# Optimization experiments

Hardware: AMD Instinct MI355X
Metric: run time of the kernel (lower is better)

Reference implementation:

```python
import jax, jax.numpy as jnp
import numpy as np

N_HEADS = 8
THETA = 10000.0
T2 = 8  # hard-coded local window sizes from the source
F2 = 8


def _rope(x, theta=THETA):
    # x: (b, h, n, d). lucidrains RotaryEmbedding convention: interleaved pairs,
    # freqs repeated '(f 2)', rotate_half on adjacent pairs.
    n, d = x.shape[-2], x.shape[-1]
    inv_freq = 1.0 / (theta ** (jnp.arange(0, d, 2, dtype=jnp.float32) / d))  # (d/2,)
    ang = jnp.arange(n, dtype=jnp.float32)[:, None] * inv_freq               # (n, d/2)
    ang = jnp.repeat(ang, 2, axis=-1)                                        # (n, d)
    cos, sin = jnp.cos(ang).astype(x.dtype), jnp.sin(ang).astype(x.dtype)
    xp = x.reshape(*x.shape[:-1], d // 2, 2)
    xr = jnp.stack([-xp[..., 1], xp[..., 0]], axis=-1).reshape(x.shape)
    return x * cos + xr * sin


def _sdpa(q, k, v):
    # non-causal scaled dot-product attention, scale = 1/sqrt(head_dim)
    d = q.shape[-1]
    s = jnp.einsum('bhqd,bhkd->bhqk', q, k) / jnp.sqrt(jnp.asarray(d, q.dtype))
    return jnp.einsum('bhqk,bhkd->bhqd', jax.nn.softmax(s, axis=-1), v)


def _attend(x, W, h):
    # x: (b, n, D); W: (D, 3D) pre-transposed Linear weight. RoPE on q and k.
    b, n, D = x.shape
    qkv = (x @ W).reshape(b, n, 3, h, D // h).transpose(2, 0, 3, 1, 4)  # (3,b,h,n,hd)
    q, k, v = _rope(qkv[0]), _rope(qkv[1]), qkv[2]
    o = _sdpa(q, k, v)  # (b, h, n, hd)
    return o.transpose(0, 2, 1, 3).reshape(b, n, D)


def reference(x, W1, W2, W3, Wp):
    B, D, T, F = x.shape
    h = N_HEADS
    # stage 1: attention along time axis, independent per (batch, freq)
    xt = x.transpose(0, 3, 2, 1).reshape(B * F, T, D)   # 'b d t f -> (b f) t d'
    xt = _attend(xt, W1, h)
    # stage 2: attention along freq axis, independent per (batch, time)
    xf = xt.reshape(B, F, T, D).transpose(0, 2, 1, 3).reshape(B * T, F, D)
    xf = _attend(xf, W2, h)
    t1, f1 = T // T2, F // F2
    xw = xf.reshape(B, t1, T2, f1, F2, D).transpose(0, 1, 3, 2, 4, 5)
    xw = xw.reshape(B * t1 * f1, T2 * F2, D)
    xw = _attend(xw, W3, h)
    y = xw.reshape(B, t1, f1, T2, F2, D).transpose(0, 1, 3, 2, 4, 5).reshape(B, T, F, D)
    y = y @ Wp                                          # c_proj, no bias
    return y.transpose(0, 3, 1, 2)                      # 'b t f d -> b d t f'


def setup_inputs() -> dict:
    key = jax.random.key(0)
    B, D, T, F = 4, 256, 256, 64
    ks = jax.random.split(key, 5)
    s = 1.0 / np.sqrt(D)
    return {
        'x': jax.random.normal(ks[0], (B, D, T, F), dtype=jnp.float32),
        'W1': jax.random.normal(ks[1], (D, 3 * D), dtype=jnp.float32) * s,
        'W2': jax.random.normal(ks[2], (D, 3 * D), dtype=jnp.float32) * s,
        'W3': jax.random.normal(ks[3], (D, 3 * D), dtype=jnp.float32) * s,
        'Wp': jax.random.normal(ks[4], (D, D), dtype=jnp.float32) * s,
    }
```

## Files before the change

### kernel.cpp

```cpp
#include <hip/hip_runtime.h>
#include <math.h>

#define B_  4
#define D_  256
#define T_  256
#define F_  64
#define H_  8

#define LN10000 9.210340371976184f
#define SM_SCALE 0.17677669529663687f
#define LOG2E    1.4426950408889634f

typedef float f32x4  __attribute__((ext_vector_type(4)));
typedef float f32x16 __attribute__((ext_vector_type(16)));
typedef short s16x8  __attribute__((ext_vector_type(8)));

__device__ __forceinline__ unsigned short f2bf(float x) {
    unsigned u = __float_as_uint(x);
    return (unsigned short)((u + 0x7fffu + ((u >> 16) & 1u)) >> 16);
}
__device__ __forceinline__ float bf2f(unsigned short h) {
    return __uint_as_float(((unsigned)h) << 16);
}
__device__ __forceinline__ int cvt_pk_bf16(float a, float b) {
    int r;
    asm("v_cvt_pk_bf16_f32 %0, %1, %2" : "=v"(r) : "v"(a), "v"(b));
    return r;
}
__device__ __forceinline__ float exp2fast(float x) {
    float r;
    asm("v_exp_f32 %0, %1" : "=v"(r) : "v"(x));
    return r;
}

__device__ __forceinline__ int xcd_swz(int lin, int nwg) {
    return (lin & 7) * (nwg >> 3) + (lin >> 3);
}

#define GLOAD_LDS(g, l)                                                         \
    __builtin_amdgcn_global_load_lds(                                           \
        (const __attribute__((address_space(1))) void*)(g),                     \
        (__attribute__((address_space(3))) void*)(l), 16, 0, 0)

__global__ __launch_bounds__(256) void rope_table(float2* __restrict__ tab) {
    const int idx = blockIdx.x * 256 + threadIdx.x;
    const int pos = idx >> 4, pr = idx & 15;
    const float freq = __expf(-(float)(2 * pr) * (LN10000 / 32.0f));
    float s, c;
    __sincosf((float)pos * freq, &s, &c);
    tab[idx] = make_float2(c, s);
}

__global__ __launch_bounds__(256) void split_w(const float* __restrict__ W,
                                               char* __restrict__ img, int N) {
    __shared__ float Wt[64][132];
    const int nb = blockIdx.x, ks = blockIdx.y;
    const int tid = threadIdx.x;
#pragma unroll
    for (int j = 0; j < 8; ++j) {
        int idx = j * 1024 + tid * 4;
        int r = idx >> 7, cidx = idx & 127;
        const float4 v = *reinterpret_cast<const float4*>(
            &W[(size_t)(ks * 64 + r) * N + nb * 128 + cidx]);
        Wt[r][cidx] = v.x; Wt[r][cidx + 1] = v.y;
        Wt[r][cidx + 2] = v.z; Wt[r][cidx + 3] = v.w;
    }
    __syncthreads();
    char* base = img + ((size_t)(nb * 4 + ks)) * 32768;
#pragma unroll
    for (int i = 0; i < 4; ++i) {
        int p = i * 256 + tid;
        int n = p >> 3, seg = p & 7;
        s16x8 hi, lo;
#pragma unroll
        for (int e = 0; e < 8; ++e) {
            float v = Wt[seg * 8 + e][n];
            unsigned short hb = f2bf(v);
            hi[e] = (short)hb;
            lo[e] = (short)f2bf(v - bf2f(hb));
        }
        int off = n * 128 + ((seg * 16) ^ ((n & 7) << 4));
        *(s16x8*)(base + off) = hi;
        *(s16x8*)(base + 16384 + off) = lo;
    }
}

__global__ __launch_bounds__(256) void transpose_in(const float* __restrict__ x,
                                                    char* __restrict__ Ximg) {
    __shared__ float tile[32][33];
    const int bt = blockIdx.z, b = bt >> 8, t = bt & 255;
    const int d0 = blockIdx.x * 32, f0 = blockIdx.y * 32;
    const int tx = threadIdx.x, ty = threadIdx.y;
    const size_t xbase = (size_t)b * D_ * T_ * F_ + (size_t)t * F_;
#pragma unroll
    for (int j = 0; j < 4; ++j) {
        int d = d0 + ty + j * 8;
        tile[ty + j * 8][tx] = x[xbase + (size_t)d * T_ * F_ + f0 + tx];
    }
    __syncthreads();
    const int tok = (b * 64 + f0 + tx) * 256 + t;
    const int rloc = tok & 127;
    const int hl = ty >> 2, seg = ty & 3;
    if (hl) return;
    char* base = Ximg + ((size_t)((tok >> 7) * 4 + (d0 >> 6))) * 32768;
    const int off = rloc * 128 + ((((d0 & 32) << 1) + seg * 16) ^ ((rloc & 7) << 4));
    s16x8 v;
#pragma unroll
    for (int e = 0; e < 8; ++e) v[e] = (short)f2bf(tile[seg * 8 + e][tx]);
    *(s16x8*)(base + off) = v;
}

__global__ __launch_bounds__(256) void gemm_x2(const char* __restrict__ Aimg,
                                               const char* __restrict__ Bimg,
                                               unsigned short* __restrict__ C, int N) {
    __shared__ alignas(16) char lds[49152];
    const int tid = threadIdx.x, lane = tid & 63, wave = tid >> 6;
    const int wm = wave >> 1, wn = wave & 1;
    const int rlo = lane & 15, rg = lane >> 4;
    const int wg = xcd_swz(blockIdx.x, gridDim.x);
    const int ncol = N >> 7;
    const int brow = wg / ncol, bcol = wg % ncol;
    f32x4 acc[4][4] = {};
    for (int ks = 0; ks < 4; ++ks) {
        const char* ga = Aimg + ((size_t)(brow * 4 + ks)) * 32768 + wave * 4096 + lane * 16;
        const char* gb = Bimg + ((size_t)(bcol * 4 + ks)) * 32768 + wave * 8192 + lane * 16;
#pragma unroll
        for (int i = 0; i < 4; ++i)
            GLOAD_LDS(ga + i * 1024, lds + wave * 4096 + lane * 16 + i * 1024);
#pragma unroll
        for (int i = 0; i < 8; ++i)
            GLOAD_LDS(gb + i * 1024, lds + 16384 + wave * 8192 + lane * 16 + i * 1024);
        __syncthreads();
#pragma unroll
        for (int kk = 0; kk < 2; ++kk) {
            s16x8 ah[4], bh[4], bl[4];
#pragma unroll
            for (int i = 0; i < 4; ++i) {
                const int ra = wm * 64 + i * 16 + rlo;
                const int ka = (kk * 64 + rg * 16) ^ ((ra & 7) << 4);
                ah[i] = *(const s16x8*)(lds + ra * 128 + ka);
                const int rb = wn * 64 + i * 16 + rlo;
                const int kb = (kk * 64 + rg * 16) ^ ((rb & 7) << 4);
                bh[i] = *(const s16x8*)(lds + 16384 + rb * 128 + kb);
                bl[i] = *(const s16x8*)(lds + 32768 + rb * 128 + kb);
            }
#pragma unroll
            for (int mt = 0; mt < 4; ++mt)
#pragma unroll
                for (int nt = 0; nt < 4; ++nt) {
                    acc[mt][nt] = __builtin_amdgcn_mfma_f32_16x16x32_bf16(ah[mt], bh[nt], acc[mt][nt], 0, 0, 0);
                    acc[mt][nt] = __builtin_amdgcn_mfma_f32_16x16x32_bf16(ah[mt], bl[nt], acc[mt][nt], 0, 0, 0);
                }
        }
        __syncthreads();
    }
    const int row0 = brow * 128 + wm * 64, col0 = bcol * 128 + wn * 64;
#pragma unroll
    for (int mt = 0; mt < 4; ++mt)
#pragma unroll
        for (int nt = 0; nt < 4; ++nt)
#pragma unroll
            for (int r = 0; r < 4; ++r)
                C[(size_t)(row0 + mt * 16 + rg * 4 + r) * N + col0 + nt * 16 + rlo] =
                    f2bf(acc[mt][nt][r]);
}

__global__ __launch_bounds__(256) void gemm_cproj(const char* __restrict__ Aimg,
                                                  const char* __restrict__ Bimg,
                                                  float* __restrict__ out, int tok0) {
    __shared__ alignas(16) char lds[65536];
    const int tid = threadIdx.x, lane = tid & 63, wave = tid >> 6;
    const int wm = wave >> 1, wn = wave & 1;
    const int rlo = lane & 15, rg = lane >> 4;
    const int wg = xcd_swz(blockIdx.x, gridDim.x);
    const int brow = wg >> 1, bcol = wg & 1;
    f32x4 acc[4][4] = {};
    for (int ks = 0; ks < 4; ++ks) {
        const char* ga = Aimg + ((size_t)(brow * 4 + ks)) * 32768 + wave * 8192 + lane * 16;
        const char* gb = Bimg + ((size_t)(bcol * 4 + ks)) * 32768 + wave * 8192 + lane * 16;
        char* la = lds + wave * 8192;
        char* lb = lds + 32768 + wave * 8192;
#pragma unroll
        for (int i = 0; i < 8; ++i) {
            GLOAD_LDS(ga + i * 1024, la + lane * 16 + i * 1024);
            GLOAD_LDS(gb + i * 1024, lb + lane * 16 + i * 1024);
        }
        __syncthreads();
#pragma unroll
        for (int kk = 0; kk < 2; ++kk) {
            s16x8 ah[4], al[4], bh[4], bl[4];
#pragma unroll
            for (int i = 0; i < 4; ++i) {
                const int ra = wm * 64 + i * 16 + rlo;
                const int ka = (kk * 64 + rg * 16) ^ ((ra & 7) << 4);
                ah[i] = *(const s16x8*)(lds + ra * 128 + ka);
                al[i] = *(const s16x8*)(lds + 16384 + ra * 128 + ka);
                const int rb = wn * 64 + i * 16 + rlo;
                const int kb = (kk * 64 + rg * 16) ^ ((rb & 7) << 4);
                bh[i] = *(const s16x8*)(lds + 32768 + rb * 128 + kb);
                bl[i] = *(const s16x8*)(lds + 49152 + rb * 128 + kb);
            }
#pragma unroll
            for (int mt = 0; mt < 4; ++mt)
#pragma unroll
                for (int nt = 0; nt < 4; ++nt) {
                    acc[mt][nt] = __builtin_amdgcn_mfma_f32_16x16x32_bf16(ah[mt], bh[nt], acc[mt][nt], 0, 0, 0);
                    acc[mt][nt] = __builtin_amdgcn_mfma_f32_16x16x32_bf16(ah[mt], bl[nt], acc[mt][nt], 0, 0, 0);
                    acc[mt][nt] = __builtin_amdgcn_mfma_f32_16x16x32_bf16(al[mt], bh[nt], acc[mt][nt], 0, 0, 0);
                }
        }
        __syncthreads();
    }
    float* ct = (float*)lds;
#pragma unroll
    for (int mt = 0; mt < 4; ++mt)
#pragma unroll
        for (int nt = 0; nt < 4; ++nt)
#pragma unroll
            for (int r = 0; r < 4; ++r) {
                const int tok = wm * 64 + mt * 16 + rg * 4 + r;
                const int d   = wn * 64 + nt * 16 + rlo;
                ct[d * 128 + (tok ^ ((d & 7) << 2))] = acc[mt][nt][r];
            }
    __syncthreads();
    const int tokb = tok0 + brow * 128;
    const int bidx = tokb >> 14;
    const int t0 = (tokb >> 6) & 255;
    const int dcol0 = bcol * 128;
#pragma unroll
    for (int it = 0; it < 16; ++it) {
        const int seg = it * 16 + (tid >> 4);
        const int dd = seg >> 1, tt = seg & 1;
        const int f0 = (tid & 15) * 4;
        const float4 v = *(const float4*)&ct[dd * 128 + ((tt * 64 + f0) ^ ((dd & 7) << 2))];
        *(float4*)&out[((size_t)((bidx * 256 + dcol0 + dd) * 256 + t0 + tt)) * 64 + f0] = v;
    }
}

template <int STAGE, bool WLO>
__global__ __launch_bounds__(256) void attn_mfma(const unsigned short* __restrict__ qkv,
                                                 char* __restrict__ Ximg,
                                                 const float2* __restrict__ ropeT, int s0) {
    constexpr int L   = (STAGE == 1) ? 256 : 64;
    constexpr int HPB = (STAGE == 1) ? 1 : 2;
    constexpr int GX  = (STAGE == 1) ? 8 : 4;
    constexpr int NCH = L / 32;
    constexpr int KVB = L * 64;
    __shared__ alignas(16) char kvLds[HPB * 2 * KVB];
    __shared__ alignas(16) float Osc[4][32][36];
    const int tid = threadIdx.x, lane = tid & 63, wave = tid >> 6;
    const int hiSel = lane >> 5;
    const int qloc = lane & 31;
    const int wg = xcd_swz(blockIdx.x, gridDim.x);
    const int hx = wg & (GX - 1);
    const int sl = wg / GX;
    float* PL = &Osc[wave][0][0];

    {
        const int nIter = (STAGE == 1) ? 2 : 1;
#pragma unroll
        for (int it = 0; it < nIter; ++it) {
            int idx, headl;
            if (STAGE == 1) { idx = it * 256 + tid; headl = 0; }
            else            { idx = tid & 127;      headl = tid >> 7; }
            const int k = idx >> 1, dh = idx & 1;
            const int h = hx * HPB + headl;
            const size_t grow = ((size_t)(sl * L + k)) * 768 + h * 32 + dh * 16;
            const s16x8 kr0 = *(const s16x8*)&qkv[grow + 256];
            const s16x8 kr1 = *(const s16x8*)&qkv[grow + 264];
            const s16x8 vr0 = *(const s16x8*)&qkv[grow + 512];
            const s16x8 vr1 = *(const s16x8*)&qkv[grow + 520];
            float kvv[16];
#pragma unroll
            for (int e = 0; e < 8; ++e) {
                kvv[e]     = bf2f((unsigned short)kr0[e]);
                kvv[8 + e] = bf2f((unsigned short)kr1[e]);
            }
#pragma unroll
            for (int j = 0; j < 8; ++j) {
                const float2 cs = ropeT[k * 16 + dh * 8 + j];
                const float x0 = kvv[2 * j], x1 = kvv[2 * j + 1];
                kvv[2 * j]     = x0 * cs.x - x1 * cs.y;
                kvv[2 * j + 1] = x1 * cs.x + x0 * cs.y;
            }
            char* kf = kvLds + headl * 2 * KVB;
            s16x8 wlo, whi;
#pragma unroll
            for (int e = 0; e < 8; ++e) {
                wlo[e] = (short)f2bf(kvv[e]);
                whi[e] = (short)f2bf(kvv[8 + e]);
            }
            *(s16x8*)(kf + (((k >> 5) * 2 + dh) * 64 + (k & 31)) * 16) = wlo;
            *(s16x8*)(kf + (((k >> 5) * 2 + dh) * 64 + 32 + (k & 31)) * 16) = whi;
            char* vf = kf + KVB;
            const int kb = k >> 4, hi8 = (k >> 3) & 1, eo = (k & 7) * 2;
#pragma unroll
            for (int dp = 0; dp < 16; ++dp) {
                const unsigned short vv = (unsigned short)((dp < 8) ? vr0[dp] : vr1[dp - 8]);
                *(unsigned short*)(vf + (kb * 64 + dh * 16 + dp + 32 * hi8) * 16 + eo) = vv;
            }
        }
    }
    __syncthreads();

    const int headl = (STAGE == 1) ? 0 : (wave >> 1);
    const int h = hx * HPB + headl;
    const char* Kf = kvLds + headl * 2 * KVB;
    const char* Vf = Kf + KVB;
    const int nPass = (STAGE == 1) ? 2 : 1;
    const float QS = SM_SCALE * LOG2E;
    const float THR = 8.0f * LOG2E;

    for (int pass = 0; pass < nPass; ++pass) {
        const int qt = (STAGE == 1) ? (wave + pass * 4) : (wave & 1);
        const int q = qt * 32 + qloc;
        s16x8 qf0, qf1;
        {
            const size_t qrow = ((size_t)(sl * L + q)) * 768 + h * 32;
            const s16x8 qr0 = *(const s16x8*)&qkv[qrow + hiSel * 8];
            const s16x8 qr1 = *(const s16x8*)&qkv[qrow + 16 + hiSel * 8];
#pragma unroll
            for (int j = 0; j < 4; ++j) {
                const float2 c0 = ropeT[q * 16 + hiSel * 4 + j];
                const float a0 = bf2f((unsigned short)qr0[2 * j]);
                const float a1 = bf2f((unsigned short)qr0[2 * j + 1]);
                qf0[2 * j]     = (short)f2bf((a0 * c0.x - a1 * c0.y) * QS);
                qf0[2 * j + 1] = (short)f2bf((a1 * c0.x + a0 * c0.y) * QS);
                const float2 c1 = ropeT[q * 16 + 8 + hiSel * 4 + j];
                const float b0 = bf2f((unsigned short)qr1[2 * j]);
                const float b1 = bf2f((unsigned short)qr1[2 * j + 1]);
                qf1[2 * j]     = (short)f2bf((b0 * c1.x - b1 * c1.y) * QS);
                qf1[2 * j + 1] = (short)f2bf((b1 * c1.x + b0 * c1.y) * QS);
            }
        }
        f32x16 o = (f32x16)0.0f;
        float m = -INFINITY, lsum = 0.f;
#pragma unroll
        for (int c = 0; c < NCH; ++c) {
            const s16x8 ka = *(const s16x8*)(Kf + (c * 2 + 0) * 1024 + lane * 16);
            const s16x8 kb = *(const s16x8*)(Kf + (c * 2 + 1) * 1024 + lane * 16);
            f32x16 S = (f32x16)0.0f;
            S = __builtin_amdgcn_mfma_f32_32x32x16_bf16(ka, qf0, S, 0, 0, 0);
            S = __builtin_amdgcn_mfma_f32_32x32x16_bf16(kb, qf1, S, 0, 0, 0);
            float cmax = S[0];
#pragma unroll
            for (int r = 1; r < 16; ++r) cmax = fmaxf(cmax, S[r]);
            cmax = fmaxf(cmax, __shfl_xor(cmax, 32, 64));
            if (__any(cmax > m + THR)) {
                const float mnew = fmaxf(m, cmax);
                const float corr = exp2fast(m - mnew);
                m = mnew;
                lsum *= corr;
#pragma unroll
                for (int r = 0; r < 16; ++r) o[r] *= corr;
            }
            float p[16], ssum = 0.f;
#pragma unroll
            for (int r = 0; r < 16; ++r) { p[r] = exp2fast(S[r] - m); ssum += p[r]; }
            lsum += ssum;
#pragma unroll
            for (int j = 0; j < 8; ++j)
                PL[((j & 1) + 4 * (j >> 1) + 2 * hiSel) * 32 + qloc] =
                    __int_as_float(cvt_pk_bf16(p[2 * j], p[2 * j + 1]));
            union { int u[4]; s16x8 v; } P0, P1;
#pragma unroll
            for (int i = 0; i < 4; ++i) {
                P0.u[i] = __float_as_int(PL[(hiSel * 4 + i) * 32 + qloc]);
                P1.u[i] = __float_as_int(PL[(8 + hiSel * 4 + i) * 32 + qloc]);
            }
            const s16x8 va = *(const s16x8*)(Vf + (c * 2 + 0) * 1024 + lane * 16);
            const s16x8 vb = *(const s16x8*)(Vf + (c * 2 + 1) * 1024 + lane * 16);
            o = __builtin_amdgcn_mfma_f32_32x32x16_bf16(va, P0.v, o, 0, 0, 0);
            o = __builtin_amdgcn_mfma_f32_32x32x16_bf16(vb, P1.v, o, 0, 0, 0);
        }
        lsum += __shfl_xor(lsum, 32, 64);
        const float inv = 1.0f / lsum;
#pragma unroll
        for (int r = 0; r < 16; ++r)
            Osc[wave][qloc][(r & 3) + 8 * (r >> 2) + 4 * hiSel] = o[r] * inv;
        int tok;
        if constexpr (STAGE == 1) {
            const int s = s0 + sl, b = s >> 6, f = s & 63;
            tok = (b * 256 + q) * 64 + f;
        } else if constexpr (STAGE == 2) {
            const int s2 = s0 + sl, b = s2 >> 8, t = s2 & 255;
            tok = ((b * 32 + (t >> 3)) * 8 + (q >> 3)) * 64 + (t & 7) * 8 + (q & 7);
        } else {
            const int w = s0 + sl, b = w >> 8, tb = (w >> 3) & 31, fb = w & 7;
            tok = (b * 256 + tb * 8 + (q >> 3)) * 64 + fb * 8 + (q & 7);
        }
        const int rloc = tok & 127;
        char* base = Ximg + ((size_t)((tok >> 7) * 4 + (h >> 1))) * 32768;
        const int sw = (rloc & 7) << 4;
        const int hb64 = (h & 1) * 64;
#pragma unroll
        for (int gg = 0; gg < 2; ++gg) {
            const int g = hiSel * 2 + gg;
            float v8[8];
            *(float4*)&v8[0] = *(const float4*)&Osc[wave][qloc][g * 8];
            *(float4*)&v8[4] = *(const float4*)&Osc[wave][qloc][g * 8 + 4];
            const int off = rloc * 128 + ((hb64 + g * 16) ^ sw);
            s16x8 hi;
#pragma unroll
            for (int e = 0; e < 8; ++e) hi[e] = (short)f2bf(v8[e]);
            *(s16x8*)(base + off) = hi;
            if constexpr (WLO) {
                s16x8 lo;
#pragma unroll
                for (int e = 0; e < 8; ++e)
                    lo[e] = (short)f2bf(v8[e] - bf2f((unsigned short)hi[e]));
                *(s16x8*)(base + 16384 + off) = lo;
            }
        }
    }
}

extern "C" void kernel_launch(void* const* d_in, const int* in_sizes, int n_in,
                              void* d_out, int out_size, void* d_ws, size_t ws_size,
                              hipStream_t stream) {
    const float* x  = (const float*)d_in[0];
    const float* W1 = (const float*)d_in[1];
    const float* W2 = (const float*)d_in[2];
    const float* W3 = (const float*)d_in[3];
    const float* Wp = (const float*)d_in[4];
    float* out = (float*)d_out;

    const size_t M = (size_t)B_ * T_ * F_;
    char* Xa = (char*)d_out;
    char* Xb = (char*)d_ws;
    char* W1i = (char*)d_ws + M * 1024;
    char* W2i = W1i + 786432;
    char* W3i = W2i + 786432;
    char* Wpi = W3i + 786432;
    float2* ropeT = (float2*)(Wpi + 262144);
    unsigned short* qkvB = (unsigned short*)((char*)ropeT + 32768);

    const size_t fixedBytes = M * 1024 + 3 * 786432 + 262144 + 32768;
    int CH = 2048;
    const int cands[5] = {65536, 32768, 16384, 8192, 4096};
    for (int i = 0; i < 5; ++i) {
        if (fixedBytes + (size_t)cands[i] * 1536 <= ws_size) { CH = cands[i]; break; }
    }
    const int NC = (int)(M / CH);

    rope_table<<<16, 256, 0, stream>>>(ropeT);
    split_w<<<dim3(6, 4), 256, 0, stream>>>(W1, W1i, 768);
    split_w<<<dim3(6, 4), 256, 0, stream>>>(W2, W2i, 768);
    split_w<<<dim3(6, 4), 256, 0, stream>>>(W3, W3i, 768);
    split_w<<<dim3(2, 4), 256, 0, stream>>>(Wp, Wpi, 256);

    transpose_in<<<dim3(8, 2, 1024), dim3(32, 8), 0, stream>>>(x, Xa);

    for (int c = 0; c < NC; ++c) {
        gemm_x2<<<(CH / 128) * 6, 256, 0, stream>>>(
            Xa + (size_t)c * CH * 1024, W1i, qkvB, 768);
        attn_mfma<1, false><<<8 * (CH / 256), 256, 0, stream>>>(
            qkvB, Xb, ropeT, c * (CH / 256));
    }
    for (int c = 0; c < NC; ++c) {
        gemm_x2<<<(CH / 128) * 6, 256, 0, stream>>>(
            Xb + (size_t)c * CH * 1024, W2i, qkvB, 768);
        attn_mfma<2, false><<<4 * (CH / 64), 256, 0, stream>>>(
            qkvB, Xa, ropeT, c * (CH / 64));
    }
    for (int c = 0; c < NC; ++c) {
        gemm_x2<<<(CH / 128) * 6, 256, 0, stream>>>(
            Xa + (size_t)c * CH * 1024, W3i, qkvB, 768);
        attn_mfma<3, true><<<4 * (CH / 64), 256, 0, stream>>>(
            qkvB, Xb, ropeT, c * (CH / 64));
    }
    for (int c = 0; c < NC; ++c) {
        gemm_cproj<<<(CH / 128) * 2, 256, 0, stream>>>(
            Xb + (size_t)c * CH * 1024, Wpi, out, c * CH);
    }
}
```

Measured before the change: 359.5 us.

## Store QKV in per-sequence head-section layout and tree-reduce softmax max/sum

The QKV GEMM epilogue now writes its output in a [seq][head][q/k/v][token][32] layout instead of row-major 768-wide rows, and the attention kernels read Q, K and V from those contiguous per-head sections. This aims to make attention loads contiguous per head and sequence, improving cache-line use. The GEMM stores become scattered 2-byte writes with more index arithmetic. Separately, the row max and row sum over 16 score values become balanced trees to shorten the dependency chain.

```diff
diff --git a/kernel.cpp b/kernel.cpp
--- a/kernel.cpp
+++ b/kernel.cpp
@@ -31,6 +31,23 @@
     float r;
     asm("v_exp_f32 %0, %1" : "=v"(r) : "v"(x));
     return r;
+}
+__device__ __forceinline__ float max16(const f32x16& S) {
+    float a0 = fmaxf(S[0], S[1]),  a1 = fmaxf(S[2], S[3]);
+    float a2 = fmaxf(S[4], S[5]),  a3 = fmaxf(S[6], S[7]);
+    float a4 = fmaxf(S[8], S[9]),  a5 = fmaxf(S[10], S[11]);
+    float a6 = fmaxf(S[12], S[13]), a7 = fmaxf(S[14], S[15]);
+    float b0 = fmaxf(a0, a1), b1 = fmaxf(a2, a3);
+    float b2 = fmaxf(a4, a5), b3 = fmaxf(a6, a7);
+    return fmaxf(fmaxf(b0, b1), fmaxf(b2, b3));
+}
+__device__ __forceinline__ float sum16(const float* p) {
+    float a0 = p[0] + p[1],  a1 = p[2] + p[3];
+    float a2 = p[4] + p[5],  a3 = p[6] + p[7];
+    float a4 = p[8] + p[9],  a5 = p[10] + p[11];
+    float a6 = p[12] + p[13], a7 = p[14] + p[15];
+    float b0 = a0 + a1, b1 = a2 + a3, b2 = a4 + a5, b3 = a6 + a7;
+    return (b0 + b1) + (b2 + b3);
 }
 
 __device__ __forceinline__ int xcd_swz(int lin, int nwg) {
@@ -110,16 +127,16 @@
     *(s16x8*)(base + off) = v;
 }
 
+template <int LSH>
 __global__ __launch_bounds__(256) void gemm_x2(const char* __restrict__ Aimg,
                                                const char* __restrict__ Bimg,
-                                               unsigned short* __restrict__ C, int N) {
+                                               unsigned short* __restrict__ C) {
     __shared__ alignas(16) char lds[49152];
     const int tid = threadIdx.x, lane = tid & 63, wave = tid >> 6;
     const int wm = wave >> 1, wn = wave & 1;
     const int rlo = lane & 15, rg = lane >> 4;
     const int wg = xcd_swz(blockIdx.x, gridDim.x);
-    const int ncol = N >> 7;
-    const int brow = wg / ncol, bcol = wg % ncol;
+    const int brow = wg / 6, bcol = wg % 6;
     f32x4 acc[4][4] = {};
     for (int ks = 0; ks < 4; ++ks) {
         const char* ga = Aimg + ((size_t)(brow * 4 + ks)) * 32768 + wave * 4096 + lane * 16;
@@ -156,13 +173,21 @@
     }
     const int row0 = brow * 128 + wm * 64, col0 = bcol * 128 + wn * 64;
 #pragma unroll
-    for (int mt = 0; mt < 4; ++mt)
-#pragma unroll
-        for (int nt = 0; nt < 4; ++nt)
-#pragma unroll
-            for (int r = 0; r < 4; ++r)
-                C[(size_t)(row0 + mt * 16 + rg * 4 + r) * N + col0 + nt * 16 + rlo] =
-                    f2bf(acc[mt][nt][r]);
+    for (int nt = 0; nt < 4; ++nt) {
+        const int col = col0 + nt * 16 + rlo;
+        const int third = col >> 8, head = (col >> 5) & 7, d = col & 31;
+        const int sec = head * 3 + third;
+#pragma unroll
+        for (int mt = 0; mt < 4; ++mt)
+#pragma unroll
+            for (int r = 0; r < 4; ++r) {
+                const int R = row0 + mt * 16 + rg * 4 + r;
+                const int seq = R >> LSH, k = R & ((1 << LSH) - 1);
+                const size_t off =
+                    ((((size_t)(seq * 24 + sec)) << LSH) + k) * 32 + d;
+                C[off] = f2bf(acc[mt][nt][r]);
+            }
+    }
 }
 
 __global__ __launch_bounds__(256) void gemm_cproj(const char* __restrict__ Aimg,
@@ -265,11 +290,11 @@
             else            { idx = tid & 127;      headl = tid >> 7; }
             const int k = idx >> 1, dh = idx & 1;
             const int h = hx * HPB + headl;
-            const size_t grow = ((size_t)(sl * L + k)) * 768 + h * 32 + dh * 16;
-            const s16x8 kr0 = *(const s16x8*)&qkv[grow + 256];
-            const s16x8 kr1 = *(const s16x8*)&qkv[grow + 264];
-            const s16x8 vr0 = *(const s16x8*)&qkv[grow + 512];
-            const s16x8 vr1 = *(const s16x8*)&qkv[grow + 520];
+            const size_t secBase = (((size_t)(sl * 8 + h) * 3) << ((STAGE == 1) ? 8 : 6)) * 32;
+            const s16x8 kr0 = *(const s16x8*)&qkv[secBase + (size_t)(L + k) * 32 + dh * 16];
+            const s16x8 kr1 = *(const s16x8*)&qkv[secBase + (size_t)(L + k) * 32 + dh * 16 + 8];
+            const s16x8 vr0 = *(const s16x8*)&qkv[secBase + (size_t)(2 * L + k) * 32 + dh * 16];
+            const s16x8 vr1 = *(const s16x8*)&qkv[secBase + (size_t)(2 * L + k) * 32 + dh * 16 + 8];
             float kvv[16];
 #pragma unroll
             for (int e = 0; e < 8; ++e) {
@@ -310,13 +335,14 @@
     const int nPass = (STAGE == 1) ? 2 : 1;
     const float QS = SM_SCALE * LOG2E;
     const float THR = 8.0f * LOG2E;
+    const size_t qSec = (((size_t)(sl * 8 + h) * 3) << ((STAGE == 1) ? 8 : 6)) * 32;
 
     for (int pass = 0; pass < nPass; ++pass) {
         const int qt = (STAGE == 1) ? (wave + pass * 4) : (wave & 1);
         const int q = qt * 32 + qloc;
         s16x8 qf0, qf1;
         {
-            const size_t qrow = ((size_t)(sl * L + q)) * 768 + h * 32;
+            const size_t qrow = qSec + (size_t)q * 32;
             const s16x8 qr0 = *(const s16x8*)&qkv[qrow + hiSel * 8];
             const s16x8 qr1 = *(const s16x8*)&qkv[qrow + 16 + hiSel * 8];
 #pragma unroll
@@ -342,9 +368,7 @@
             f32x16 S = (f32x16)0.0f;
             S = __builtin_amdgcn_mfma_f32_32x32x16_bf16(ka, qf0, S, 0, 0, 0);
             S = __builtin_amdgcn_mfma_f32_32x32x16_bf16(kb, qf1, S, 0, 0, 0);
-            float cmax = S[0];
-#pragma unroll
-            for (int r = 1; r < 16; ++r) cmax = fmaxf(cmax, S[r]);
+            float cmax = max16(S);
             cmax = fmaxf(cmax, __shfl_xor(cmax, 32, 64));
             if (__any(cmax > m + THR)) {
                 const float mnew = fmaxf(m, cmax);
@@ -354,10 +378,10 @@
 #pragma unroll
                 for (int r = 0; r < 16; ++r) o[r] *= corr;
             }
-            float p[16], ssum = 0.f;
-#pragma unroll
-            for (int r = 0; r < 16; ++r) { p[r] = exp2fast(S[r] - m); ssum += p[r]; }
-            lsum += ssum;
+            float p[16];
+#pragma unroll
+            for (int r = 0; r < 16; ++r) p[r] = exp2fast(S[r] - m);
+            lsum += sum16(p);
 #pragma unroll
             for (int j = 0; j < 8; ++j)
                 PL[((j & 1) + 4 * (j >> 1) + 2 * hiSel) * 32 + qloc] =
@@ -452,20 +476,20 @@
     transpose_in<<<dim3(8, 2, 1024), dim3(32, 8), 0, stream>>>(x, Xa);
 
     for (int c = 0; c < NC; ++c) {
-        gemm_x2<<<(CH / 128) * 6, 256, 0, stream>>>(
-            Xa + (size_t)c * CH * 1024, W1i, qkvB, 768);
+        gemm_x2<8><<<(CH / 128) * 6, 256, 0, stream>>>(
+            Xa + (size_t)c * CH * 1024, W1i, qkvB);
         attn_mfma<1, false><<<8 * (CH / 256), 256, 0, stream>>>(
             qkvB, Xb, ropeT, c * (CH / 256));
     }
     for (int c = 0; c < NC; ++c) {
-        gemm_x2<<<(CH / 128) * 6, 256, 0, stream>>>(
-            Xb + (size_t)c * CH * 1024, W2i, qkvB, 768);
+        gemm_x2<6><<<(CH / 128) * 6, 256, 0, stream>>>(
+            Xb + (size_t)c * CH * 1024, W2i, qkvB);
         attn_mfma<2, false><<<4 * (CH / 64), 256, 0, stream>>>(
             qkvB, Xa, ropeT, c * (CH / 64));
     }
     for (int c = 0; c < NC; ++c) {
-        gemm_x2<<<(CH / 128) * 6, 256, 0, stream>>>(
-            Xa + (size_t)c * CH * 1024, W3i, qkvB, 768);
+        gemm_x2<6><<<(CH / 128) * 6, 256, 0, stream>>>(
+            Xa + (size_t)c * CH * 1024, W3i, qkvB);
         attn_mfma<3, true><<<4 * (CH / 64), 256, 0, stream>>>(
             qkvB, Xb, ropeT, c * (CH / 64));
     }
```

Result: no change. 356.0 us (-1.0%).
